# Performance work log

Hardware: AMD Instinct MI355X
Metric: run time of the kernel (lower is better)

The kernel has to match this reference:

```python
import jax, jax.numpy as jnp
import numpy as np

M = 7            # window_size
NUM_HEADS = 12
C = 384
D_HEAD = C // NUM_HEADS
SCALE = D_HEAD ** (-0.5)


def _relative_position_index(m):
    coords = np.stack(np.meshgrid(np.arange(m), np.arange(m), indexing='ij')).reshape(2, -1)
    rel = coords[:, :, None] - coords[:, None, :]          # [2, m^2, m^2]
    rel = rel.transpose(1, 2, 0).astype(np.int64)          # [m^2, m^2, 2]
    rel[..., 0] += m - 1
    rel[..., 1] += m - 1
    rel[..., 0] *= 2 * m - 1
    return jnp.asarray(rel.sum(-1))                         # [m^2, m^2]

REL_INDEX = _relative_position_index(M)


def setup_inputs() -> dict:
    key = jax.random.key(0)
    ks = jax.random.split(key, 7)
    B_, N = 4096, M * M
    x = jax.random.normal(ks[0], (B_, N, C), dtype=jnp.float32)
    mask = jax.random.normal(ks[1], (64, N, N), dtype=jnp.float32)
    bias_table = 0.02 * jax.random.normal(ks[2], ((2 * M - 1) * (2 * M - 1), NUM_HEADS), dtype=jnp.float32)
    qkv_w = 0.02 * jax.random.normal(ks[3], (3 * C, C), dtype=jnp.float32)
    qkv_b = jnp.zeros((3 * C,), dtype=jnp.float32)
    proj_w = 0.02 * jax.random.normal(ks[4], (C, C), dtype=jnp.float32)
    proj_b = jnp.zeros((C,), dtype=jnp.float32)
    return {"x": x, "mask": mask, "bias_table": bias_table,
            "qkv_w": qkv_w, "qkv_b": qkv_b, "proj_w": proj_w, "proj_b": proj_b}


def reference(x, mask, bias_table, qkv_w, qkv_b, proj_w, proj_b):
    B_, N, _ = x.shape
    H, d = NUM_HEADS, D_HEAD
    qkv = x @ qkv_w.T + qkv_b                              # [B_, N, 3C]
    qkv = qkv.reshape(B_, N, 3, H, d)
    q = qkv[:, :, 0].transpose(0, 2, 1, 3)                 # [B_, H, N, d]
    k = qkv[:, :, 1].transpose(0, 2, 1, 3)
    v = qkv[:, :, 2].transpose(0, 2, 1, 3)
    attn = jnp.einsum('bhnd,bhmd->bhnm', q, k) * SCALE     # [B_, H, N, N]
    bias = bias_table[REL_INDEX.reshape(-1)].reshape(N, N, H).transpose(2, 0, 1)
    attn = attn + bias[None]
    nW = mask.shape[0]
    attn = attn.reshape(B_ // nW, nW, H, N, N) + mask[None, :, None]
    attn = attn.reshape(B_, H, N, N)
    attn = jax.nn.softmax(attn, axis=-1)
    out = jnp.einsum('bhnm,bhmd->bhnd', attn, v)           # [B_, H, N, d]
    out = out.transpose(0, 2, 1, 3).reshape(B_, N, C)
    return out @ proj_w.T + proj_b
```

## Files before the change

kernel.cpp:

```cpp
#include <hip/hip_runtime.h>
#include <stdint.h>

typedef __attribute__((ext_vector_type(8))) short bf16x8;
typedef __attribute__((ext_vector_type(4))) short bf16x4;
typedef __attribute__((ext_vector_type(4))) float f32x4;
typedef __attribute__((ext_vector_type(2))) unsigned int u32x2;

#define NSCALE 0.17677669529663687f

static __device__ __forceinline__ float bf2f(unsigned short h) {
  union { unsigned int u; float f; } c; c.u = ((unsigned int)h) << 16; return c.f;
}
static __device__ __forceinline__ unsigned short f2bf(float f) {
  union { float f; unsigned int u; } c; c.f = f;
  unsigned int u = c.u;
  u = (u + 0x7FFFu + ((u >> 16) & 1u)) >> 16;
  return (unsigned short)u;
}
static __device__ __forceinline__ unsigned int packbf2(float a, float b) {
  return (unsigned int)f2bf(a) | ((unsigned int)f2bf(b) << 16);
}

#define W_QKVW  0
#define W_PROJW 442368
#define W_BIASE 589824
#define W_ELEMS 619240
#define W_BYTES (W_ELEMS * 2)

__global__ void cvt_w_kernel(const float* __restrict__ qkv_w,
                             const float* __restrict__ proj_w,
                             unsigned short* __restrict__ ws) {
  const int i = blockIdx.x * 256 + threadIdx.x;
  const int stride = gridDim.x * 256;
  for (int e = i; e < 442368; e += stride)
    ws[W_QKVW + e] = f2bf(qkv_w[e] * (e < 147456 ? NSCALE : 1.f));
  for (int e = i; e < 147456; e += stride)
    ws[W_PROJW + e] = f2bf(proj_w[e]);
}

__global__ void biase_kernel(const float* __restrict__ bias_t,
                             unsigned short* __restrict__ ws) {
  const int h = blockIdx.x;
  unsigned short* dst = ws + W_BIASE + h * 2450;
  for (int e = threadIdx.x; e < 2401; e += 256) {
    const int q = e / 49, k = e - q * 49;
    const int i1 = q / 7, j1 = q - i1 * 7;
    const int i2 = k / 7, j2 = k - i2 * 7;
    const int ridx = (i1 - i2 + 6) * 13 + (j1 - j2 + 6);
    dst[q * 50 + k] = f2bf(bias_t[ridx * 12 + h]);
  }
}

#define XS_O  0
#define U_O   19208
#define QS_O  (U_O)
#define KS_O  (U_O + 3920)
#define VT_O  (U_O + 7840)
#define MSP_O (U_O + 12448)
#define LDS_EL (U_O + 12448 + 2458)
#define LDS_BYTES2 (LDS_EL * 2)

__global__ void __launch_bounds__(256)
__attribute__((amdgpu_waves_per_eu(2, 4)))
winattn11(const float* __restrict__ x,
          const float* __restrict__ mask,
          const float* __restrict__ qkv_b,
          const float* __restrict__ proj_b,
          const unsigned short* __restrict__ ws,
          float* __restrict__ out)
{
  extern __shared__ unsigned short sm[];
  unsigned short* Xs  = sm + XS_O;
  unsigned short* Qs  = sm + QS_O;
  unsigned short* Ks  = sm + KS_O;
  unsigned short* Vt  = sm + VT_O;
  unsigned short* Msp = sm + MSP_O;
  unsigned short* Os  = sm + XS_O;

  const unsigned short* wsQW = ws + W_QKVW;
  const unsigned short* wsPW = ws + W_PROJW;
  const unsigned short* wsBE = ws + W_BIASE;

  const int b = blockIdx.x;
  const int tid = threadIdx.x;
  const int w = tid >> 6, lane = tid & 63, l15 = lane & 15, lg = lane >> 4;

  const float* xw = x + b * 18816;
  for (int e = tid; e < 4704; e += 256) {
    const int f = e << 2;
    const int r = f / 384;
    const int c = f - r * 384;
    f32x4 v = *(const f32x4*)(xw + f);
    u32x2 pk; pk[0] = packbf2(v[0], v[1]); pk[1] = packbf2(v[2], v[3]);
    *(u32x2*)(Xs + r * 392 + c) = pk;
  }
  {
    const float* mw = mask + (b & 63) * 2401;
    for (int e = tid; e < 2401; e += 256) {
      const int q = e / 49, k = e - q * 49;
      Msp[q * 50 + k] = f2bf(mw[e]);
    }
  }
  __syncthreads();

  const int q  = w * 16 + l15;
  const int qc = q > 48 ? 48 : q;

  unsigned int opk[6][2][2][2];

  for (int g = 0; g < 6; ++g) {
    const int hb = 2 * g;
    {
      const int ntb = 3 * w;
      const unsigned short* bp[3];
      float bias[3];
#pragma unroll
      for (int i = 0; i < 3; ++i) {
        const int nt = ntb + i;
        const int s = nt >> 2, sub = nt & 3, hh = sub >> 1, hf = sub & 1;
        const int o = s * 384 + (hb + hh) * 32 + hf * 16 + l15;
        bp[i] = wsQW + o * 384 + lg * 8;
        bias[i] = qkv_b[o] * (s == 0 ? NSCALE : 1.f);
      }
      f32x4 acc[3][4];
#pragma unroll
      for (int i = 0; i < 3; ++i)
#pragma unroll
        for (int mi = 0; mi < 4; ++mi) acc[i][mi] = (f32x4){0.f, 0.f, 0.f, 0.f};
#pragma unroll
      for (int kk = 0; kk < 12; ++kk) {
        bf16x8 A4[4];
#pragma unroll
        for (int mi = 0; mi < 4; ++mi) {
          const int ar = mi * 16 + l15;
          A4[mi] = *(const bf16x8*)(Xs + (ar > 48 ? 48 : ar) * 392 + kk * 32 + lg * 8);
        }
        bf16x8 B3[3];
#pragma unroll
        for (int i = 0; i < 3; ++i) B3[i] = *(const bf16x8*)(bp[i] + kk * 32);
#pragma unroll
        for (int i = 0; i < 3; ++i)
#pragma unroll
          for (int mi = 0; mi < 4; ++mi)
            acc[i][mi] = __builtin_amdgcn_mfma_f32_16x16x32_bf16(A4[mi], B3[i], acc[i][mi], 0, 0, 0);
      }
#pragma unroll
      for (int i = 0; i < 3; ++i) {
        const int nt = ntb + i;
        const int s = nt >> 2, sub = nt & 3, hh = sub >> 1, hf = sub & 1;
        if (s < 2) {
          unsigned short* T = (s == 0 ? Qs : Ks) + hh * 1960 + hf * 16 + l15;
#pragma unroll
          for (int mi = 0; mi < 4; ++mi)
#pragma unroll
            for (int j = 0; j < 4; ++j) {
              const int row = mi * 16 + lg * 4 + j;
              if (row < 49) T[row * 40] = f2bf(acc[i][mi][j] + bias[i]);
            }
        } else {
#pragma unroll
          for (int mi = 0; mi < 4; ++mi) {
            bf16x4 pk;
#pragma unroll
            for (int j = 0; j < 4; ++j) pk[j] = (short)f2bf(acc[i][mi][j] + bias[i]);
            *(bf16x4*)(Vt + hh * 2304 + (hf * 16 + l15) * 72 + mi * 16 + lg * 4) = pk;
          }
        }
      }
    }
    __syncthreads();

#pragma unroll
    for (int hh = 0; hh < 2; ++hh) {
      const int head = hb + hh;
      bf16x8 Qf = *(const bf16x8*)(Qs + hh * 1960 + qc * 40 + lg * 8);
      f32x4 S[4];
#pragma unroll
      for (int mt = 0; mt < 4; ++mt) {
        const int kr = mt * 16 + l15;
        bf16x8 Kf = *(const bf16x8*)(Ks + hh * 1960 + (kr > 48 ? 48 : kr) * 40 + lg * 8);
        f32x4 z = {0.f, 0.f, 0.f, 0.f};
        S[mt] = __builtin_amdgcn_mfma_f32_16x16x32_bf16(Kf, Qf, z, 0, 0, 0);
      }
      const unsigned short* be = wsBE + head * 2450 + qc * 50;
      const unsigned short* ms = Msp + qc * 50;
      float p[16];
      float vmax = -3e30f;
#pragma unroll
      for (int mt = 0; mt < 4; ++mt) {
        const int kc0 = mt * 16 + lg * 4;
        const int ko = kc0 > 48 ? 48 : kc0;
        const unsigned int b01 = *(const unsigned int*)(be + ko);
        const unsigned int b23 = *(const unsigned int*)(be + ko + 2);
        const unsigned int m01 = *(const unsigned int*)(ms + ko);
        const unsigned int m23 = *(const unsigned int*)(ms + ko + 2);
        float ad0 = bf2f((unsigned short)(b01 & 0xffff)) + bf2f((unsigned short)(m01 & 0xffff));
        float ad1 = bf2f((unsigned short)(b01 >> 16))    + bf2f((unsigned short)(m01 >> 16));
        float ad2 = bf2f((unsigned short)(b23 & 0xffff)) + bf2f((unsigned short)(m23 & 0xffff));
        float ad3 = bf2f((unsigned short)(b23 >> 16))    + bf2f((unsigned short)(m23 >> 16));
        float v0 = S[mt][0] + ad0, v1 = S[mt][1] + ad1;
        float v2 = S[mt][2] + ad2, v3 = S[mt][3] + ad3;
        if (kc0 + 0 >= 49) v0 = -3e30f;
        if (kc0 + 1 >= 49) v1 = -3e30f;
        if (kc0 + 2 >= 49) v2 = -3e30f;
        if (kc0 + 3 >= 49) v3 = -3e30f;
        p[mt * 4 + 0] = v0; p[mt * 4 + 1] = v1;
        p[mt * 4 + 2] = v2; p[mt * 4 + 3] = v3;
        vmax = fmaxf(fmaxf(fmaxf(v0, v1), fmaxf(v2, v3)), vmax);
      }
      vmax = fmaxf(vmax, __shfl_xor(vmax, 16, 64));
      vmax = fmaxf(vmax, __shfl_xor(vmax, 32, 64));
      float ssum = 0.f;
#pragma unroll
      for (int i = 0; i < 16; ++i) { p[i] = __expf(p[i] - vmax); ssum += p[i]; }
      ssum += __shfl_xor(ssum, 16, 64);
      ssum += __shfl_xor(ssum, 32, 64);
      const float rs = 1.f / ssum;
      unsigned int plo[4], phi[4];
#pragma unroll
      for (int mt = 0; mt < 4; ++mt) {
        plo[mt] = packbf2(p[mt * 4 + 0], p[mt * 4 + 1]);
        phi[mt] = packbf2(p[mt * 4 + 2], p[mt * 4 + 3]);
      }
      union { bf16x8 v; unsigned int u[4]; } PB[2];
      const int src0 = l15 + ((lg & 1) << 5);
      const int src1 = src0 + 16;
      const int sel = lg >> 1;
#pragma unroll
      for (int ks = 0; ks < 2; ++ks) {
        const int a0 = __shfl((int)plo[2 * ks], src0, 64), a1 = __shfl((int)plo[2 * ks + 1], src0, 64);
        const int b0 = __shfl((int)phi[2 * ks], src0, 64), b1 = __shfl((int)phi[2 * ks + 1], src0, 64);
        const int c0 = __shfl((int)plo[2 * ks], src1, 64), c1 = __shfl((int)plo[2 * ks + 1], src1, 64);
        const int d0 = __shfl((int)phi[2 * ks], src1, 64), d1 = __shfl((int)phi[2 * ks + 1], src1, 64);
        PB[ks].u[0] = (unsigned)(sel ? a1 : a0);
        PB[ks].u[1] = (unsigned)(sel ? b1 : b0);
        PB[ks].u[2] = (unsigned)(sel ? c1 : c0);
        PB[ks].u[3] = (unsigned)(sel ? d1 : d0);
      }
#pragma unroll
      for (int dt = 0; dt < 2; ++dt) {
        f32x4 a = {0.f, 0.f, 0.f, 0.f};
#pragma unroll
        for (int ks = 0; ks < 2; ++ks) {
          bf16x8 Vf = *(const bf16x8*)(Vt + hh * 2304 + (dt * 16 + l15) * 72 + ks * 32 + lg * 8);
          a = __builtin_amdgcn_mfma_f32_16x16x32_bf16(Vf, PB[ks].v, a, 0, 0, 0);
        }
        const unsigned int lo = packbf2(a[0] * rs, a[1] * rs);
        const unsigned int hi = packbf2(a[2] * rs, a[3] * rs);
        switch (g) {
          case 0: opk[0][hh][dt][0] = lo; opk[0][hh][dt][1] = hi; break;
          case 1: opk[1][hh][dt][0] = lo; opk[1][hh][dt][1] = hi; break;
          case 2: opk[2][hh][dt][0] = lo; opk[2][hh][dt][1] = hi; break;
          case 3: opk[3][hh][dt][0] = lo; opk[3][hh][dt][1] = hi; break;
          case 4: opk[4][hh][dt][0] = lo; opk[4][hh][dt][1] = hi; break;
          default: opk[5][hh][dt][0] = lo; opk[5][hh][dt][1] = hi; break;
        }
      }
    }
    __syncthreads();
  }

  if (q < 49) {
#pragma unroll
    for (int gg = 0; gg < 6; ++gg)
#pragma unroll
      for (int hh = 0; hh < 2; ++hh)
#pragma unroll
        for (int dt = 0; dt < 2; ++dt) {
          u32x2 pk; pk[0] = opk[gg][hh][dt][0]; pk[1] = opk[gg][hh][dt][1];
          *(u32x2*)(Os + q * 392 + (2 * gg + hh) * 32 + dt * 16 + lg * 4) = pk;
        }
  }
  __syncthreads();

  {
    float* ob = out + (size_t)b * 18816;
#pragma unroll
    for (int pp = 0; pp < 2; ++pp) {
      const unsigned short* bp[3];
      float pb[3];
      int co[3];
#pragma unroll
      for (int i = 0; i < 3; ++i) {
        co[i] = (6 * w + 3 * pp + i) * 16 + l15;
        bp[i] = wsPW + co[i] * 384 + lg * 8;
        pb[i] = proj_b[co[i]];
      }
      f32x4 acc[3][4];
#pragma unroll
      for (int i = 0; i < 3; ++i)
#pragma unroll
        for (int mi = 0; mi < 4; ++mi) acc[i][mi] = (f32x4){0.f, 0.f, 0.f, 0.f};
#pragma unroll
      for (int kk = 0; kk < 12; ++kk) {
        bf16x8 A4[4];
#pragma unroll
        for (int mi = 0; mi < 4; ++mi) {
          const int ar = mi * 16 + l15;
          A4[mi] = *(const bf16x8*)(Os + (ar > 48 ? 48 : ar) * 392 + kk * 32 + lg * 8);
        }
        bf16x8 B3[3];
#pragma unroll
        for (int i = 0; i < 3; ++i) B3[i] = *(const bf16x8*)(bp[i] + kk * 32);
#pragma unroll
        for (int i = 0; i < 3; ++i)
#pragma unroll
          for (int mi = 0; mi < 4; ++mi)
            acc[i][mi] = __builtin_amdgcn_mfma_f32_16x16x32_bf16(A4[mi], B3[i], acc[i][mi], 0, 0, 0);
      }
#pragma unroll
      for (int i = 0; i < 3; ++i)
#pragma unroll
        for (int mi = 0; mi < 4; ++mi)
#pragma unroll
          for (int j = 0; j < 4; ++j) {
            const int row = mi * 16 + lg * 4 + j;
            if (row < 49) ob[row * 384 + co[i]] = acc[i][mi][j] + pb[i];
          }
    }
  }
}

#define FXS 0
#define FQS (FXS + 64*392)
#define FKS (FQS + 2*64*40)
#define FVT (FKS + 2*64*40)
#define FPS (FVT + 2*32*72)
#define FOS (FPS + 2*64*72)
#define FMS (FOS + 64*392)
#define FBS (FMS + 2408)
#define FLDS_EL (FBS + 2028)
#define FLDS_BYTES (FLDS_EL * 2)

static __device__ __forceinline__ bf16x8 cvt8(const float* p) {
  f32x4 a = *(const f32x4*)p;
  f32x4 b = *(const f32x4*)(p + 4);
  bf16x8 r;
  r[0]=(short)f2bf(a[0]); r[1]=(short)f2bf(a[1]); r[2]=(short)f2bf(a[2]); r[3]=(short)f2bf(a[3]);
  r[4]=(short)f2bf(b[0]); r[5]=(short)f2bf(b[1]); r[6]=(short)f2bf(b[2]); r[7]=(short)f2bf(b[3]);
  return r;
}

__global__ __launch_bounds__(512, 2)
void winattn_fb(const float* __restrict__ x, const float* __restrict__ mask,
                const float* __restrict__ bias_t, const float* __restrict__ qkv_w,
                const float* __restrict__ qkv_b, const float* __restrict__ proj_w,
                const float* __restrict__ proj_b, float* __restrict__ out)
{
  extern __shared__ unsigned short sm[];
  unsigned short* Xs = sm + FXS; unsigned short* Qs = sm + FQS;
  unsigned short* Ks = sm + FKS; unsigned short* Vt = sm + FVT;
  unsigned short* Ps = sm + FPS; unsigned short* Os = sm + FOS;
  unsigned short* Ms = sm + FMS; unsigned short* Bs = sm + FBS;
  const int b = blockIdx.x, tid = threadIdx.x;
  const int w = tid >> 6, lane = tid & 63, l15 = lane & 15, lg = lane >> 4;
  const float* xw = x + b * 18816;
  for (int e = tid; e < 4704; e += 512) {
    const int f = e << 2; const int r = f / 384; const int c = f - r * 384;
    f32x4 v = *(const f32x4*)(xw + f);
    unsigned short* dst = Xs + r * 392 + c;
    dst[0]=f2bf(v[0]); dst[1]=f2bf(v[1]); dst[2]=f2bf(v[2]); dst[3]=f2bf(v[3]);
  }
  { bf16x8 z = {0,0,0,0,0,0,0,0};
    for (int e = tid; e < 735; e += 512) *(bf16x8*)(Xs + 19208 + (e << 3)) = z; }
  { const float* mw = mask + (b & 63) * 2401;
    for (int e = tid; e < 2401; e += 512) Ms[e] = f2bf(mw[e]);
    for (int e = tid; e < 2028; e += 512) Bs[e] = f2bf(bias_t[e]); }
  __syncthreads();
  for (int g = 0; g < 6; ++g) {
    int t = 6 * w; const int tEnd = t + 6;
    while (t < tEnd) {
      const int nt = t >> 2; const int hh = nt / 6; const int ntl = nt - hh * 6;
      const int s = ntl >> 1; const int dd = ((nt & 1) << 4) + l15;
      const int o = s * 384 + (2 * g + hh) * 32 + dd;
      bf16x8 Bf[12];
      const float* wp = qkv_w + o * 384 + lg * 8;
#pragma unroll
      for (int kk = 0; kk < 12; ++kk) Bf[kk] = cvt8(wp + kk * 32);
      const float biasc = qkv_b[o];
      for (; t < tEnd && (t >> 2) == nt; ++t) {
        const int mt = t & 3;
        f32x4 acc = {0.f,0.f,0.f,0.f};
        const unsigned short* ap = Xs + (mt * 16 + l15) * 392 + lg * 8;
#pragma unroll
        for (int kk = 0; kk < 12; ++kk) {
          bf16x8 Af = *(const bf16x8*)(ap + kk * 32);
          acc = __builtin_amdgcn_mfma_f32_16x16x32_bf16(Af, Bf[kk], acc, 0,0,0);
        }
#pragma unroll
        for (int j = 0; j < 4; ++j) {
          const int row = mt * 16 + lg * 4 + j;
          const unsigned short hv = f2bf(acc[j] + biasc);
          if (s == 0) Qs[hh * 2560 + row * 40 + dd] = hv;
          else if (s == 1) Ks[hh * 2560 + row * 40 + dd] = hv;
          else Vt[hh * 2304 + dd * 72 + row] = hv;
        }
      }
    }
    __syncthreads();
    {
      const int hh = w >> 2; const int mt = w & 3; const int head = 2 * g + hh;
      bf16x8 Aq = *(const bf16x8*)(Qs + hh * 2560 + (mt * 16 + l15) * 40 + lg * 8);
      f32x4 accs[4];
#pragma unroll
      for (int nt = 0; nt < 4; ++nt) {
        bf16x8 Bk = *(const bf16x8*)(Ks + hh * 2560 + (nt * 16 + l15) * 40 + lg * 8);
        f32x4 z = {0.f,0.f,0.f,0.f};
        accs[nt] = __builtin_amdgcn_mfma_f32_16x16x32_bf16(Aq, Bk, z, 0,0,0);
      }
#pragma unroll
      for (int j = 0; j < 4; ++j) {
        const int row = mt * 16 + lg * 4 + j;
        float sv[4]; float vmax = -3e30f;
#pragma unroll
        for (int nt = 0; nt < 4; ++nt) {
          const int col = nt * 16 + l15;
          float v = accs[nt][j] * NSCALE;
          if (col < 49) { if (row < 49) {
              const int i1 = row / 7, j1 = row - i1 * 7;
              const int i2 = col / 7, j2 = col - i2 * 7;
              const int ridx = (i1 - i2 + 6) * 13 + (j1 - j2 + 6);
              v += bf2f(Ms[row * 49 + col]) + bf2f(Bs[ridx * 12 + head]); } }
          else v = -3e30f;
          sv[nt] = v; vmax = fmaxf(vmax, v);
        }
#pragma unroll
        for (int mm = 1; mm < 16; mm <<= 1) vmax = fmaxf(vmax, __shfl_xor(vmax, mm, 64));
        float ssum = 0.f;
#pragma unroll
        for (int nt = 0; nt < 4; ++nt) { sv[nt] = __expf(sv[nt] - vmax); ssum += sv[nt]; }
#pragma unroll
        for (int mm = 1; mm < 16; mm <<= 1) ssum += __shfl_xor(ssum, mm, 64);
        const float rs = 1.f / ssum;
#pragma unroll
        for (int nt = 0; nt < 4; ++nt)
          Ps[hh * 4608 + row * 72 + nt * 16 + l15] = f2bf(sv[nt] * rs);
      }
    }
    __syncthreads();
    {
      const int hh = w >> 2; const int mt = w & 3; const int head = 2 * g + hh;
#pragma unroll
      for (int nt = 0; nt < 2; ++nt) {
        f32x4 acc = {0.f,0.f,0.f,0.f};
#pragma unroll
        for (int kk = 0; kk < 2; ++kk) {
          bf16x8 Ap = *(const bf16x8*)(Ps + hh * 4608 + (mt * 16 + l15) * 72 + kk * 32 + lg * 8);
          bf16x8 Bv = *(const bf16x8*)(Vt + hh * 2304 + (nt * 16 + l15) * 72 + kk * 32 + lg * 8);
          acc = __builtin_amdgcn_mfma_f32_16x16x32_bf16(Ap, Bv, acc, 0,0,0);
        }
#pragma unroll
        for (int j = 0; j < 4; ++j)
          Os[(mt * 16 + lg * 4 + j) * 392 + head * 32 + nt * 16 + l15] = f2bf(acc[j]);
      }
    }
    __syncthreads();
  }
  for (int nt = 3 * w; nt < 3 * w + 3; ++nt) {
    const int co = nt * 16 + l15;
    bf16x8 Bf[12];
    const float* wp = proj_w + co * 384 + lg * 8;
#pragma unroll
    for (int kk = 0; kk < 12; ++kk) Bf[kk] = cvt8(wp + kk * 32);
    const float pb = proj_b[co];
#pragma unroll
    for (int mt = 0; mt < 4; ++mt) {
      f32x4 acc = {0.f,0.f,0.f,0.f};
      const unsigned short* ap = Os + (mt * 16 + l15) * 392 + lg * 8;
#pragma unroll
      for (int kk = 0; kk < 12; ++kk) {
        bf16x8 Af = *(const bf16x8*)(ap + kk * 32);
        acc = __builtin_amdgcn_mfma_f32_16x16x32_bf16(Af, Bf[kk], acc, 0,0,0);
      }
#pragma unroll
      for (int j = 0; j < 4; ++j) {
        const int row = mt * 16 + lg * 4 + j;
        if (row < 49) out[b * 18816 + row * 384 + co] = acc[j] + pb;
      }
    }
  }
}

extern "C" void kernel_launch(void* const* d_in, const int* in_sizes, int n_in,
                              void* d_out, int out_size, void* d_ws, size_t ws_size,
                              hipStream_t stream) {
  const float* x      = (const float*)d_in[0];
  const float* mask   = (const float*)d_in[1];
  const float* bias_t = (const float*)d_in[2];
  const float* qkv_w  = (const float*)d_in[3];
  const float* qkv_b  = (const float*)d_in[4];
  const float* proj_w = (const float*)d_in[5];
  const float* proj_b = (const float*)d_in[6];
  float* out = (float*)d_out;

  if (ws_size >= (size_t)W_BYTES) {
    unsigned short* ws = (unsigned short*)d_ws;
    cvt_w_kernel<<<dim3(1024), dim3(256), 0, stream>>>(qkv_w, proj_w, ws);
    biase_kernel<<<dim3(12), dim3(256), 0, stream>>>(bias_t, ws);
    (void)hipFuncSetAttribute((const void*)winattn11,
                              hipFuncAttributeMaxDynamicSharedMemorySize, LDS_BYTES2);
    winattn11<<<dim3(4096), dim3(256), LDS_BYTES2, stream>>>(
        x, mask, qkv_b, proj_b, ws, out);
  } else {
    (void)hipFuncSetAttribute((const void*)winattn_fb,
                              hipFuncAttributeMaxDynamicSharedMemorySize, FLDS_BYTES);
    winattn_fb<<<dim3(4096), dim3(512), FLDS_BYTES, stream>>>(
        x, mask, bias_t, qkv_w, qkv_b, proj_w, proj_b, out);
  }
}
```

Before: 753.7 us.

## Process one head per iteration and precompute bf16 mask to shrink LDS

```diff
diff --git a/kernel.cpp b/kernel.cpp
--- a/kernel.cpp
+++ b/kernel.cpp
@@ -24,7 +24,8 @@
 #define W_QKVW  0
 #define W_PROJW 442368
 #define W_BIASE 589824
-#define W_ELEMS 619240
+#define W_MASKE 619224
+#define W_ELEMS 776024
 #define W_BYTES (W_ELEMS * 2)
 
 __global__ void cvt_w_kernel(const float* __restrict__ qkv_w,
@@ -51,35 +52,44 @@
   }
 }
 
+__global__ void maske_kernel(const float* __restrict__ mask,
+                             unsigned short* __restrict__ ws) {
+  const int wn = blockIdx.x;
+  const float* mw = mask + wn * 2401;
+  unsigned short* dst = ws + W_MASKE + wn * 2450;
+  for (int e = threadIdx.x; e < 2401; e += 256) {
+    const int q = e / 49, k = e - q * 49;
+    dst[q * 50 + k] = f2bf(mw[e]);
+  }
+}
+
 #define XS_O  0
 #define U_O   19208
 #define QS_O  (U_O)
-#define KS_O  (U_O + 3920)
-#define VT_O  (U_O + 7840)
-#define MSP_O (U_O + 12448)
-#define LDS_EL (U_O + 12448 + 2458)
+#define KS_O  (U_O + 1960)
+#define VT_O  (U_O + 3920)
+#define LDS_EL (U_O + 6224)
 #define LDS_BYTES2 (LDS_EL * 2)
 
 __global__ void __launch_bounds__(256)
 __attribute__((amdgpu_waves_per_eu(2, 4)))
-winattn11(const float* __restrict__ x,
-          const float* __restrict__ mask,
+winattn12(const float* __restrict__ x,
           const float* __restrict__ qkv_b,
           const float* __restrict__ proj_b,
           const unsigned short* __restrict__ ws,
           float* __restrict__ out)
 {
   extern __shared__ unsigned short sm[];
-  unsigned short* Xs  = sm + XS_O;
-  unsigned short* Qs  = sm + QS_O;
-  unsigned short* Ks  = sm + KS_O;
-  unsigned short* Vt  = sm + VT_O;
-  unsigned short* Msp = sm + MSP_O;
-  unsigned short* Os  = sm + XS_O;
+  unsigned short* Xs = sm + XS_O;
+  unsigned short* Qs = sm + QS_O;
+  unsigned short* Ks = sm + KS_O;
+  unsigned short* Vt = sm + VT_O;
+  unsigned short* Os = sm + XS_O;
 
   const unsigned short* wsQW = ws + W_QKVW;
   const unsigned short* wsPW = ws + W_PROJW;
   const unsigned short* wsBE = ws + W_BIASE;
+  const unsigned short* wsME = ws + W_MASKE;
 
   const int b = blockIdx.x;
   const int tid = threadIdx.x;
@@ -94,46 +104,42 @@
     u32x2 pk; pk[0] = packbf2(v[0], v[1]); pk[1] = packbf2(v[2], v[3]);
     *(u32x2*)(Xs + r * 392 + c) = pk;
   }
-  {
-    const float* mw = mask + (b & 63) * 2401;
-    for (int e = tid; e < 2401; e += 256) {
-      const int q = e / 49, k = e - q * 49;
-      Msp[q * 50 + k] = f2bf(mw[e]);
-    }
-  }
   __syncthreads();
 
+  const int tq = w >> 1;
+  const int mh = w & 1;
   const int q  = w * 16 + l15;
   const int qc = q > 48 ? 48 : q;
-
-  unsigned int opk[6][2][2][2];
-
-  for (int g = 0; g < 6; ++g) {
-    const int hb = 2 * g;
+  const unsigned short* mebase = wsME + (b & 63) * 2450 + qc * 50;
+
+  unsigned int opk[12][2][2];
+
+  for (int g = 0; g < 12; ++g) {
     {
-      const int ntb = 3 * w;
       const unsigned short* bp[3];
       float bias[3];
+      int ss[3], hf_[3];
 #pragma unroll
       for (int i = 0; i < 3; ++i) {
-        const int nt = ntb + i;
-        const int s = nt >> 2, sub = nt & 3, hh = sub >> 1, hf = sub & 1;
-        const int o = s * 384 + (hb + hh) * 32 + hf * 16 + l15;
+        const int nt = 3 * tq + i;
+        const int s = nt >> 1, hf = nt & 1;
+        const int o = s * 384 + g * 32 + hf * 16 + l15;
         bp[i] = wsQW + o * 384 + lg * 8;
         bias[i] = qkv_b[o] * (s == 0 ? NSCALE : 1.f);
-      }
-      f32x4 acc[3][4];
+        ss[i] = s; hf_[i] = hf;
+      }
+      f32x4 acc[3][2];
 #pragma unroll
       for (int i = 0; i < 3; ++i)
 #pragma unroll
-        for (int mi = 0; mi < 4; ++mi) acc[i][mi] = (f32x4){0.f, 0.f, 0.f, 0.f};
+        for (int mi = 0; mi < 2; ++mi) acc[i][mi] = (f32x4){0.f, 0.f, 0.f, 0.f};
 #pragma unroll
       for (int kk = 0; kk < 12; ++kk) {
-        bf16x8 A4[4];
-#pragma unroll
-        for (int mi = 0; mi < 4; ++mi) {
-          const int ar = mi * 16 + l15;
-          A4[mi] = *(const bf16x8*)(Xs + (ar > 48 ? 48 : ar) * 392 + kk * 32 + lg * 8);
+        bf16x8 A2[2];
+#pragma unroll
+        for (int mi = 0; mi < 2; ++mi) {
+          const int ar = (2 * mh + mi) * 16 + l15;
+          A2[mi] = *(const bf16x8*)(Xs + (ar > 48 ? 48 : ar) * 392 + kk * 32 + lg * 8);
         }
         bf16x8 B3[3];
 #pragma unroll
@@ -141,49 +147,45 @@
 #pragma unroll
         for (int i = 0; i < 3; ++i)
 #pragma unroll
-          for (int mi = 0; mi < 4; ++mi)
-            acc[i][mi] = __builtin_amdgcn_mfma_f32_16x16x32_bf16(A4[mi], B3[i], acc[i][mi], 0, 0, 0);
+          for (int mi = 0; mi < 2; ++mi)
+            acc[i][mi] = __builtin_amdgcn_mfma_f32_16x16x32_bf16(A2[mi], B3[i], acc[i][mi], 0, 0, 0);
       }
 #pragma unroll
       for (int i = 0; i < 3; ++i) {
-        const int nt = ntb + i;
-        const int s = nt >> 2, sub = nt & 3, hh = sub >> 1, hf = sub & 1;
+        const int s = ss[i], hf = hf_[i];
         if (s < 2) {
-          unsigned short* T = (s == 0 ? Qs : Ks) + hh * 1960 + hf * 16 + l15;
-#pragma unroll
-          for (int mi = 0; mi < 4; ++mi)
+          unsigned short* T = (s == 0 ? Qs : Ks) + hf * 16 + l15;
+#pragma unroll
+          for (int mi = 0; mi < 2; ++mi)
 #pragma unroll
             for (int j = 0; j < 4; ++j) {
-              const int row = mi * 16 + lg * 4 + j;
+              const int row = (2 * mh + mi) * 16 + lg * 4 + j;
               if (row < 49) T[row * 40] = f2bf(acc[i][mi][j] + bias[i]);
             }
         } else {
 #pragma unroll
-          for (int mi = 0; mi < 4; ++mi) {
+          for (int mi = 0; mi < 2; ++mi) {
             bf16x4 pk;
 #pragma unroll
             for (int j = 0; j < 4; ++j) pk[j] = (short)f2bf(acc[i][mi][j] + bias[i]);
-            *(bf16x4*)(Vt + hh * 2304 + (hf * 16 + l15) * 72 + mi * 16 + lg * 4) = pk;
+            *(bf16x4*)(Vt + (hf * 16 + l15) * 72 + (2 * mh + mi) * 16 + lg * 4) = pk;
           }
         }
       }
     }
     __syncthreads();
 
-#pragma unroll
-    for (int hh = 0; hh < 2; ++hh) {
-      const int head = hb + hh;
-      bf16x8 Qf = *(const bf16x8*)(Qs + hh * 1960 + qc * 40 + lg * 8);
+    {
+      bf16x8 Qf = *(const bf16x8*)(Qs + qc * 40 + lg * 8);
       f32x4 S[4];
 #pragma unroll
       for (int mt = 0; mt < 4; ++mt) {
         const int kr = mt * 16 + l15;
-        bf16x8 Kf = *(const bf16x8*)(Ks + hh * 1960 + (kr > 48 ? 48 : kr) * 40 + lg * 8);
+        bf16x8 Kf = *(const bf16x8*)(Ks + (kr > 48 ? 48 : kr) * 40 + lg * 8);
         f32x4 z = {0.f, 0.f, 0.f, 0.f};
         S[mt] = __builtin_amdgcn_mfma_f32_16x16x32_bf16(Kf, Qf, z, 0, 0, 0);
       }
-      const unsigned short* be = wsBE + head * 2450 + qc * 50;
-      const unsigned short* ms = Msp + qc * 50;
+      const unsigned short* be = wsBE + g * 2450 + qc * 50;
       float p[16];
       float vmax = -3e30f;
 #pragma unroll
@@ -192,8 +194,8 @@
         const int ko = kc0 > 48 ? 48 : kc0;
         const unsigned int b01 = *(const unsigned int*)(be + ko);
         const unsigned int b23 = *(const unsigned int*)(be + ko + 2);
-        const unsigned int m01 = *(const unsigned int*)(ms + ko);
-        const unsigned int m23 = *(const unsigned int*)(ms + ko + 2);
+        const unsigned int m01 = *(const unsigned int*)(mebase + ko);
+        const unsigned int m23 = *(const unsigned int*)(mebase + ko + 2);
         float ad0 = bf2f((unsigned short)(b01 & 0xffff)) + bf2f((unsigned short)(m01 & 0xffff));
         float ad1 = bf2f((unsigned short)(b01 >> 16))    + bf2f((unsigned short)(m01 >> 16));
         float ad2 = bf2f((unsigned short)(b23 & 0xffff)) + bf2f((unsigned short)(m23 & 0xffff));
@@ -242,18 +244,24 @@
         f32x4 a = {0.f, 0.f, 0.f, 0.f};
 #pragma unroll
         for (int ks = 0; ks < 2; ++ks) {
-          bf16x8 Vf = *(const bf16x8*)(Vt + hh * 2304 + (dt * 16 + l15) * 72 + ks * 32 + lg * 8);
+          bf16x8 Vf = *(const bf16x8*)(Vt + (dt * 16 + l15) * 72 + ks * 32 + lg * 8);
           a = __builtin_amdgcn_mfma_f32_16x16x32_bf16(Vf, PB[ks].v, a, 0, 0, 0);
         }
         const unsigned int lo = packbf2(a[0] * rs, a[1] * rs);
         const unsigned int hi = packbf2(a[2] * rs, a[3] * rs);
         switch (g) {
-          case 0: opk[0][hh][dt][0] = lo; opk[0][hh][dt][1] = hi; break;
-          case 1: opk[1][hh][dt][0] = lo; opk[1][hh][dt][1] = hi; break;
-          case 2: opk[2][hh][dt][0] = lo; opk[2][hh][dt][1] = hi; break;
-          case 3: opk[3][hh][dt][0] = lo; opk[3][hh][dt][1] = hi; break;
-          case 4: opk[4][hh][dt][0] = lo; opk[4][hh][dt][1] = hi; break;
-          default: opk[5][hh][dt][0] = lo; opk[5][hh][dt][1] = hi; break;
+          case 0:  opk[0][dt][0]  = lo; opk[0][dt][1]  = hi; break;
+          case 1:  opk[1][dt][0]  = lo; opk[1][dt][1]  = hi; break;
+          case 2:  opk[2][dt][0]  = lo; opk[2][dt][1]  = hi; break;
+          case 3:  opk[3][dt][0]  = lo; opk[3][dt][1]  = hi; break;
+          case 4:  opk[4][dt][0]  = lo; opk[4][dt][1]  = hi; break;
+          case 5:  opk[5][dt][0]  = lo; opk[5][dt][1]  = hi; break;
+          case 6:  opk[6][dt][0]  = lo; opk[6][dt][1]  = hi; break;
+          case 7:  opk[7][dt][0]  = lo; opk[7][dt][1]  = hi; break;
+          case 8:  opk[8][dt][0]  = lo; opk[8][dt][1]  = hi; break;
+          case 9:  opk[9][dt][0]  = lo; opk[9][dt][1]  = hi; break;
+          case 10: opk[10][dt][0] = lo; opk[10][dt][1] = hi; break;
+          default: opk[11][dt][0] = lo; opk[11][dt][1] = hi; break;
         }
       }
     }
@@ -262,14 +270,12 @@
 
   if (q < 49) {
 #pragma unroll
-    for (int gg = 0; gg < 6; ++gg)
-#pragma unroll
-      for (int hh = 0; hh < 2; ++hh)
-#pragma unroll
-        for (int dt = 0; dt < 2; ++dt) {
-          u32x2 pk; pk[0] = opk[gg][hh][dt][0]; pk[1] = opk[gg][hh][dt][1];
-          *(u32x2*)(Os + q * 392 + (2 * gg + hh) * 32 + dt * 16 + lg * 4) = pk;
-        }
+    for (int gg = 0; gg < 12; ++gg)
+#pragma unroll
+      for (int dt = 0; dt < 2; ++dt) {
+        u32x2 pk; pk[0] = opk[gg][dt][0]; pk[1] = opk[gg][dt][1];
+        *(u32x2*)(Os + q * 392 + gg * 32 + dt * 16 + lg * 4) = pk;
+      }
   }
   __syncthreads();
 
@@ -497,10 +503,11 @@
     unsigned short* ws = (unsigned short*)d_ws;
     cvt_w_kernel<<<dim3(1024), dim3(256), 0, stream>>>(qkv_w, proj_w, ws);
     biase_kernel<<<dim3(12), dim3(256), 0, stream>>>(bias_t, ws);
-    (void)hipFuncSetAttribute((const void*)winattn11,
+    maske_kernel<<<dim3(64), dim3(256), 0, stream>>>(mask, ws);
+    (void)hipFuncSetAttribute((const void*)winattn12,
                               hipFuncAttributeMaxDynamicSharedMemorySize, LDS_BYTES2);
-    winattn11<<<dim3(4096), dim3(256), LDS_BYTES2, stream>>>(
-        x, mask, qkv_b, proj_b, ws, out);
+    winattn12<<<dim3(4096), dim3(256), LDS_BYTES2, stream>>>(
+        x, qkv_b, proj_b, ws, out);
   } else {
     (void)hipFuncSetAttribute((const void*)winattn_fb,
                               hipFuncAttributeMaxDynamicSharedMemorySize, FLDS_BYTES);
```

After: 1.174 ms. 1.56x slower.
